# Optimization experiments

Measured on AMD Instinct MI355X. Metric: run time of the kernel, lower is better.

Reference implementation:

```python
import jax, jax.numpy as jnp
import numpy as np

ALPHA = 0.8
GAMMA = 2.0
SMOOTH = 1e-4
FOCAL_W = 20.0
DICE_W = 1.0
IOU_W = 1.0
MASK_THRESH = 0.0
AREA_RANGES = np.array([[0.0, 0.04], [0.01, 0.16], [0.09, 0.49], [0.25, 1.0]], dtype=np.float32)
B, K, H, W = 128, 4, 256, 256


def setup_inputs() -> dict:
    key = jax.random.key(0)
    k1, k2, k3, k4 = jax.random.split(key, 4)
    pred_masks = jax.random.normal(k1, (B, K, H, W), dtype=jnp.float32)
    pred_ious = jax.random.uniform(k2, (B, K), dtype=jnp.float32)
    # binary targets with varying per-sample foreground density so different
    # samples fall into different area_ranges (exercises the branching)
    dens = jax.random.uniform(k3, (B, 1, 1, 1), dtype=jnp.float32)
    noise = jax.random.uniform(k4, (B, 1, H, W), dtype=jnp.float32)
    targets = (noise < dens).astype(jnp.float32)
    return {"pred_masks": pred_masks, "pred_ious": pred_ious, "targets": targets}


def _aggregate(loss_bk, valid_bk):
    # per-sample mean over valid idxs, then mean over samples with >=1 valid idx
    cnt = valid_bk.sum(axis=1)                                   # [B]
    per_sample = (loss_bk * valid_bk).sum(axis=1) / jnp.maximum(cnt, 1.0)
    per_sample = jnp.where(cnt > 0, per_sample, 0.0)
    vb = (cnt > 0).astype(loss_bk.dtype).sum()
    total = per_sample.sum()
    return jnp.where(vb > 0, total / jnp.maximum(vb, 1.0), total)


def _compute(pred_masks, pred_ious, targets):
    b = pred_masks.shape[0]
    x = pred_masks.reshape(b, K, -1)                             # [B,K,HW] logits
    t = targets.reshape(b, -1)                                   # [B,HW] binary
    hw = t.shape[1]
    ratio = t.sum(axis=1) / float(hw)                            # [B]
    lo = jnp.asarray(AREA_RANGES[:, 0])
    hi = jnp.asarray(AREA_RANGES[:, 1])
    valid = ((ratio[:, None] > lo[None, :]) & (ratio[:, None] < hi[None, :])).astype(x.dtype)  # [B,K]

    tb = t[:, None, :]                                           # [B,1,HW]
    # focal: stable BCE-with-logits, elementwise
    bce = jnp.maximum(x, 0.0) - x * tb + jnp.log1p(jnp.exp(-jnp.abs(x)))
    focal_bk = (ALPHA * (1.0 - jnp.exp(-bce)) ** GAMMA * bce).mean(axis=2)  # [B,K]
    focal = FOCAL_W * _aggregate(focal_bk, valid)

    # dice on clamped sigmoid probabilities
    p = jnp.clip(jax.nn.sigmoid(x), 1e-4, 1.0 - 1e-4)
    inter = (p * tb).sum(axis=2)                                 # [B,K]
    dice_bk = 1.0 - (2.0 * inter + SMOOTH) / (p.sum(axis=2) + t.sum(axis=1)[:, None] + SMOOTH)
    dice = DICE_W * _aggregate(dice_bk, valid)

    # iou prediction loss on thresholded masks
    m = (x >= MASK_THRESH).astype(x.dtype)
    i2 = (m * tb).sum(axis=2)
    iou_gt = (i2 + SMOOTH) / (m.sum(axis=2) + t.sum(axis=1)[:, None] - i2 + SMOOTH)
    iou_bk = (pred_ious - iou_gt) ** 2                           # [B,K]
    iou = IOU_W * _aggregate(iou_bk, valid)

    return focal, dice, iou


def reference(pred_masks, pred_ious, targets):
    focal, dice, iou = _compute(pred_masks, pred_ious, targets)
    return focal, dice, iou
```

## Files before the change

kernel.cpp:

```cpp
#include <hip/hip_runtime.h>
#include <math.h>

#define B_   128
#define K_   4
#define HW_  65536

constexpr int BLOCK = 256;
constexpr int NC    = 8;
constexpr int CHUNK = HW_ / NC;
constexpr int G     = CHUNK / 4 / BLOCK;

typedef float vfloat4 __attribute__((ext_vector_type(4)));

__device__ __forceinline__ void proc_elem(float x, float t,
                                          float& fs, float& in, float& ps,
                                          float& i2, float& ms) {
    float e   = __expf(-fabsf(x));
    float inv = __builtin_amdgcn_rcpf(1.0f + e);
    bool  pos = (x >= 0.0f);
    float s   = pos ? inv : 1.0f - inv;
    float nms = fmaf(-2.0f, s, 1.0f);
    float pt  = fmaf(t, nms, s);
    float l   = __logf(pt);
    float om  = 1.0f - pt;
    fs = fmaf(om * om * l, -0.8f, fs);
    float pc  = fminf(fmaxf(s, 1e-4f), 0.9999f);
    ps += pc;
    in  = fmaf(pc, t, in);
    float m = pos ? 1.0f : 0.0f;
    ms += m;
    i2  = fmaf(m, t, i2);
}

__device__ __forceinline__ void proc4(const vfloat4& xv, const vfloat4& tv,
                                      float& fs, float& in, float& ps,
                                      float& i2, float& ms, float& ts) {
    proc_elem(xv.x, tv.x, fs, in, ps, i2, ms);
    proc_elem(xv.y, tv.y, fs, in, ps, i2, ms);
    proc_elem(xv.z, tv.z, fs, in, ps, i2, ms);
    proc_elem(xv.w, tv.w, fs, in, ps, i2, ms);
    ts += tv.x + tv.y + tv.z + tv.w;
}

__global__ __launch_bounds__(BLOCK, 8) void partial_kernel(
    const float* __restrict__ pred_masks,
    const float* __restrict__ targets,
    float* __restrict__ fsum,
    float* __restrict__ inter,
    float* __restrict__ psum,
    float* __restrict__ i2s,
    float* __restrict__ msum,
    float* __restrict__ tsum)
{
    const int blk = blockIdx.x;
    const int k   = blk & (K_ - 1);
    const int bc  = blk >> 2;
    const int c   = bc & (NC - 1);
    const int b   = bc >> 3;

    const vfloat4* __restrict__ t4 =
        reinterpret_cast<const vfloat4*>(targets + (size_t)b * HW_ + c * CHUNK);
    const vfloat4* __restrict__ x4 =
        reinterpret_cast<const vfloat4*>(pred_masks +
            ((size_t)(b * K_ + k)) * HW_ + c * CHUNK);

    float fs = 0.f, in = 0.f, ps = 0.f, i2 = 0.f, ms = 0.f, ts = 0.f;

    int idx = threadIdx.x;
    vfloat4 tA = t4[idx];
    vfloat4 xA = x4[idx];
    vfloat4 tB = t4[idx + BLOCK];
    vfloat4 xB = x4[idx + BLOCK];

    #pragma unroll 1
    for (int g = 0; g < G - 2; g += 2) {
        proc4(xA, tA, fs, in, ps, i2, ms, ts);
        tA = t4[idx + 2 * BLOCK];
        xA = x4[idx + 2 * BLOCK];
        proc4(xB, tB, fs, in, ps, i2, ms, ts);
        tB = t4[idx + 3 * BLOCK];
        xB = x4[idx + 3 * BLOCK];
        idx += 2 * BLOCK;
    }
    proc4(xA, tA, fs, in, ps, i2, ms, ts);
    proc4(xB, tB, fs, in, ps, i2, ms, ts);

    float vals[6] = {fs, in, ps, i2, ms, ts};
    const int lane = threadIdx.x & 63;
    const int wave = threadIdx.x >> 6;

    #pragma unroll
    for (int v = 0; v < 6; ++v) {
        float x = vals[v];
        #pragma unroll
        for (int off = 32; off > 0; off >>= 1) x += __shfl_down(x, off, 64);
        vals[v] = x;
    }

    __shared__ float smem[6 * 4];
    if (lane == 0) {
        #pragma unroll
        for (int v = 0; v < 6; ++v) smem[v * 4 + wave] = vals[v];
    }
    __syncthreads();

    if (threadIdx.x < 6) {
        const int v = threadIdx.x;
        const float x = smem[v * 4 + 0] + smem[v * 4 + 1] +
                        smem[v * 4 + 2] + smem[v * 4 + 3];
        const int bk = b * K_ + k;
        float* dst;
        if      (v == 0) dst = &fsum[bk];
        else if (v == 1) dst = &inter[bk];
        else if (v == 2) dst = &psum[bk];
        else if (v == 3) dst = &i2s[bk];
        else if (v == 4) dst = &msum[bk];
        else             dst = &tsum[b];
        atomicAdd(dst, x);
    }
}

__global__ __launch_bounds__(128) void finalize_kernel(
    const float* __restrict__ pred_ious,
    const float* __restrict__ fsum,
    const float* __restrict__ inter,
    const float* __restrict__ psum,
    const float* __restrict__ i2s,
    const float* __restrict__ msum,
    const float* __restrict__ tsum,
    float* __restrict__ out)
{
    const float lo[K_] = {0.00f, 0.01f, 0.09f, 0.25f};
    const float hi[K_] = {0.04f, 0.16f, 0.49f, 1.00f};
    const float SMOOTH = 0.0001f;

    const int b = threadIdx.x;
    const float ts = tsum[b] * 0.25f;
    const float ratio = ts * (1.0f / (float)HW_);

    float cnt = 0.f, fA = 0.f, dA = 0.f, iA = 0.f;
    #pragma unroll
    for (int k = 0; k < K_; ++k) {
        const bool valid = (ratio > lo[k]) && (ratio < hi[k]);
        if (valid) {
            cnt += 1.0f;
            fA += fsum[b * K_ + k] * (1.0f / (float)HW_);
            const float in_ = inter[b * K_ + k];
            const float ps_ = psum[b * K_ + k];
            dA += 1.0f - (2.0f * in_ + SMOOTH) / (ps_ + ts + SMOOTH);
            const float i2_ = i2s[b * K_ + k];
            const float ms_ = msum[b * K_ + k];
            const float gt  = (i2_ + SMOOTH) / (ms_ + ts - i2_ + SMOOTH);
            const float d   = pred_ious[b * K_ + k] - gt;
            iA += d * d;
        }
    }
    const float invc = (cnt > 0.f) ? (1.0f / cnt) : 0.0f;
    fA *= invc; dA *= invc; iA *= invc;
    float vb = (cnt > 0.f) ? 1.0f : 0.0f;

    float vals[4] = {fA, dA, iA, vb};
    const int lane = threadIdx.x & 63;
    const int wave = threadIdx.x >> 6;
    #pragma unroll
    for (int v = 0; v < 4; ++v) {
        float x = vals[v];
        #pragma unroll
        for (int off = 32; off > 0; off >>= 1) x += __shfl_down(x, off, 64);
        vals[v] = x;
    }
    __shared__ float smem[4 * 2];
    if (lane == 0) {
        #pragma unroll
        for (int v = 0; v < 4; ++v) smem[v * 2 + wave] = vals[v];
    }
    __syncthreads();
    if (threadIdx.x == 0) {
        const float fT  = smem[0] + smem[1];
        const float dT  = smem[2] + smem[3];
        const float iT  = smem[4] + smem[5];
        const float vbT = smem[6] + smem[7];
        const float scale = (vbT > 0.f) ? (1.0f / vbT) : 1.0f;
        out[0] = 20.0f * fT * scale;
        out[1] = dT * scale;
        out[2] = iT * scale;
    }
}

extern "C" void kernel_launch(void* const* d_in, const int* in_sizes, int n_in,
                              void* d_out, int out_size, void* d_ws, size_t ws_size,
                              hipStream_t stream) {
    const float* pred_masks = (const float*)d_in[0];
    const float* pred_ious  = (const float*)d_in[1];
    const float* targets    = (const float*)d_in[2];
    float* out = (float*)d_out;

    float* ws    = (float*)d_ws;
    float* fsum  = ws;
    float* inter = ws + 512;
    float* psum  = ws + 1024;
    float* i2s   = ws + 1536;
    float* msum  = ws + 2048;
    float* tsum  = ws + 2560;

    (void)hipMemsetAsync(d_ws, 0, 2688 * sizeof(float), stream);

    partial_kernel<<<B_ * NC * K_, BLOCK, 0, stream>>>(
        pred_masks, targets, fsum, inter, psum, i2s, msum, tsum);
    finalize_kernel<<<1, 128, 0, stream>>>(
        pred_ious, fsum, inter, psum, i2s, msum, tsum, out);
}
```

Measured before the change: 221.0 us.

## Remap blocks per XCD, use nontemporal logit loads, deepen prefetch to four

Halves the number of spatial chunks per sample, so each block covers twice as many elements. Block indices are remapped so that the four k-blocks sharing a target chunk, and neighbouring samples, land on the same XCD, which is meant to improve L2 reuse of the targets. Logit loads become nontemporal so they do not evict target data, and the software prefetch deepens from two to four vec4 pairs in flight, with launch bounds relaxed to fit the extra registers. Fewer blocks (2048) and lower occupancy could reduce latency hiding.

```diff
diff --git a/kernel.cpp b/kernel.cpp
--- a/kernel.cpp
+++ b/kernel.cpp
@@ -6,7 +6,7 @@
 #define HW_  65536
 
 constexpr int BLOCK = 256;
-constexpr int NC    = 8;
+constexpr int NC    = 4;
 constexpr int CHUNK = HW_ / NC;
 constexpr int G     = CHUNK / 4 / BLOCK;
 
@@ -42,7 +42,7 @@
     ts += tv.x + tv.y + tv.z + tv.w;
 }
 
-__global__ __launch_bounds__(BLOCK, 8) void partial_kernel(
+__global__ __launch_bounds__(BLOCK, 6) void partial_kernel(
     const float* __restrict__ pred_masks,
     const float* __restrict__ targets,
     float* __restrict__ fsum,
@@ -52,11 +52,12 @@
     float* __restrict__ msum,
     float* __restrict__ tsum)
 {
-    const int blk = blockIdx.x;
-    const int k   = blk & (K_ - 1);
-    const int bc  = blk >> 2;
-    const int c   = bc & (NC - 1);
-    const int b   = bc >> 3;
+    const int xcd  = blockIdx.x & 7;
+    const int seq  = blockIdx.x >> 3;
+    const int k    = seq & (K_ - 1);
+    const int pair = xcd * 64 + (seq >> 2);
+    const int b    = pair >> 2;
+    const int c    = pair & (NC - 1);
 
     const vfloat4* __restrict__ t4 =
         reinterpret_cast<const vfloat4*>(targets + (size_t)b * HW_ + c * CHUNK);
@@ -68,22 +69,34 @@
 
     int idx = threadIdx.x;
     vfloat4 tA = t4[idx];
-    vfloat4 xA = x4[idx];
+    vfloat4 xA = __builtin_nontemporal_load(&x4[idx]);
     vfloat4 tB = t4[idx + BLOCK];
-    vfloat4 xB = x4[idx + BLOCK];
+    vfloat4 xB = __builtin_nontemporal_load(&x4[idx + BLOCK]);
+    vfloat4 tC = t4[idx + 2 * BLOCK];
+    vfloat4 xC = __builtin_nontemporal_load(&x4[idx + 2 * BLOCK]);
+    vfloat4 tD = t4[idx + 3 * BLOCK];
+    vfloat4 xD = __builtin_nontemporal_load(&x4[idx + 3 * BLOCK]);
 
     #pragma unroll 1
-    for (int g = 0; g < G - 2; g += 2) {
+    for (int g = 0; g + 4 < G; g += 4) {
         proc4(xA, tA, fs, in, ps, i2, ms, ts);
-        tA = t4[idx + 2 * BLOCK];
-        xA = x4[idx + 2 * BLOCK];
+        tA = t4[idx + 4 * BLOCK];
+        xA = __builtin_nontemporal_load(&x4[idx + 4 * BLOCK]);
         proc4(xB, tB, fs, in, ps, i2, ms, ts);
-        tB = t4[idx + 3 * BLOCK];
-        xB = x4[idx + 3 * BLOCK];
-        idx += 2 * BLOCK;
+        tB = t4[idx + 5 * BLOCK];
+        xB = __builtin_nontemporal_load(&x4[idx + 5 * BLOCK]);
+        proc4(xC, tC, fs, in, ps, i2, ms, ts);
+        tC = t4[idx + 6 * BLOCK];
+        xC = __builtin_nontemporal_load(&x4[idx + 6 * BLOCK]);
+        proc4(xD, tD, fs, in, ps, i2, ms, ts);
+        tD = t4[idx + 7 * BLOCK];
+        xD = __builtin_nontemporal_load(&x4[idx + 7 * BLOCK]);
+        idx += 4 * BLOCK;
     }
     proc4(xA, tA, fs, in, ps, i2, ms, ts);
     proc4(xB, tB, fs, in, ps, i2, ms, ts);
+    proc4(xC, tC, fs, in, ps, i2, ms, ts);
+    proc4(xD, tD, fs, in, ps, i2, ms, ts);
 
     float vals[6] = {fs, in, ps, i2, ms, ts};
     const int lane = threadIdx.x & 63;
```

Result: faster. 215.4 us (-2.5%).
